# Performance work log

Measured on AMD Instinct MI355X. Metric: run time of the kernel, lower is better.

## Reference

```python
import jax, jax.numpy as jnp
import numpy as np

HEADS = 8
EPS = 1e-12  # F.normalize default eps


def conv1x1(t, w):
    # t: (B, Cin, H, W); w: (Cout, Cin) -> (B, Cout, H, W)
    return jnp.einsum('bchw,oc->bohw', t, w)


def cosine_attn(q, k, v, scale):
    # q: (B,h,d,Nq); k,v: (B,h,d,Nk). Cosine attention: L2-normalize over feature dim d.
    q = q / jnp.maximum(jnp.linalg.norm(q, axis=2, keepdims=True), EPS)
    k = k / jnp.maximum(jnp.linalg.norm(k, axis=2, keepdims=True), EPS)
    attn = jnp.einsum('bhdq,bhdk->bhqk', q, k) * scale
    attn = jax.nn.softmax(attn, axis=-1)
    return jnp.einsum('bhqk,bhdk->bhdq', attn, v)  # (B,h,d,Nq)


def setup_inputs() -> dict:
    key = jax.random.key(0)
    ks = jax.random.split(key, 8)
    B, C, H, W, L = 8, 512, 64, 64, 16
    def w(k, o, i):
        return jax.random.normal(k, (o, i), dtype=jnp.float32) * (1.0 / np.sqrt(i))
    return {
        'x': jax.random.normal(ks[0], (B, C, H, W), dtype=jnp.float32),
        'latents': jax.random.normal(ks[1], (1, C, 1, L), dtype=jnp.float32) * 0.02,
        'w_q_lat': w(ks[2], C, C),
        'w_kv_x': w(ks[3], 2 * C, C),
        'w_q_x': w(ks[4], C, C),
        'w_kv_lat': w(ks[5], 2 * C, C),
        'w_proj': w(ks[6], C, C),
        'b_proj': jnp.zeros((C,), dtype=jnp.float32),
    }


def reference(x, latents, w_q_lat, w_kv_x, w_q_x, w_kv_lat, w_proj, b_proj):
    B, C, H, W = x.shape
    L = latents.shape[-1]
    h = HEADS
    d = C // h
    scale = d ** (-0.5)

    # latents read from spatial features (compression)
    lat = jnp.broadcast_to(latents, (B, C, 1, L))
    ql = conv1x1(lat, w_q_lat).reshape(B, h, d, L)
    kvx = conv1x1(x, w_kv_x)
    kx = kvx[:, :C].reshape(B, h, d, H * W)
    vx = kvx[:, C:].reshape(B, h, d, H * W)
    lat_read = cosine_attn(ql, kx, vx, scale).reshape(B, C, 1, L)

    # latents write back into features (expansion)
    qx = conv1x1(x, w_q_x).reshape(B, h, d, H * W)
    kvl = conv1x1(lat_read, w_kv_lat)
    kl = kvl[:, :C].reshape(B, h, d, L)
    vl = kvl[:, C:].reshape(B, h, d, L)
    x_write = cosine_attn(qx, kl, vl, scale).reshape(B, C, H, W)

    # output projection (dropout p=0 -> identity)
    return conv1x1(x_write, w_proj) + b_proj[None, :, None, None]
```

## Files before the change

kernel.cpp:

```cpp
#include <hip/hip_runtime.h>


typedef __bf16 bf16x8 __attribute__((ext_vector_type(8)));
typedef float floatx4 __attribute__((ext_vector_type(4)));
typedef short short8_t __attribute__((ext_vector_type(8)));
typedef short short4_t __attribute__((ext_vector_type(4)));

#define DEV __device__ __forceinline__

DEV float bf2f(unsigned short u){ union{unsigned int i; float f;} v; v.i = ((unsigned int)u)<<16; return v.f; }
DEV unsigned short f2bf(float f){
  union{float f; unsigned int i;} v; v.f = f;
  unsigned int i = v.i;
  return (unsigned short)((i + 0x7fffu + ((i>>16)&1u)) >> 16);
}

DEV void glds16(const void* g, void* l){
  __builtin_amdgcn_global_load_lds((const __attribute__((address_space(1))) void*)g,
                                   (__attribute__((address_space(3))) void*)l, 16, 0, 0);
}

#define OFF_XT     256ull
#define OFF_KVX    (OFF_XT + 33554432ull)
#define OFF_WKVX   (OFF_KVX + 67108864ull)
#define OFF_WQX    (OFF_WKVX + 1048576ull)
#define OFF_WKVL   (OFF_WQX + 524288ull)
#define OFF_WPROJ  (OFF_WKVL + 1048576ull)
#define OFF_WQLAT  (OFF_WPROJ + 524288ull)
#define OFF_LATF   (OFF_WQLAT + 524288ull)
#define OFF_BIAS   (OFF_LATF + 32768ull)
#define OFF_QLH    (OFF_BIAS + 4096ull)
#define OFF_GNUM   (OFF_QLH + 32768ull)
#define OFF_GDEN   (OFF_GNUM + 524288ull)
#define OFF_KVL    (OFF_GDEN + 4096ull)
#define OFF_KHAT   (OFF_KVL + 524288ull)
#define OFF_GVL    (OFF_KHAT + 524288ull)

__global__ void k_sniff(const unsigned short* __restrict__ x, int* flag){
  int t = threadIdx.x;
  int m = 0;
  for (int i = t; i < 4096; i += 256){ int e = (x[i]>>7)&0xFF; m = (e>m)?e:m; }
  __shared__ int red[256];
  red[t] = m; __syncthreads();
  for (int s = 128; s > 0; s >>= 1){ if (t < s) red[t] = (red[t+s]>red[t])?red[t+s]:red[t]; __syncthreads(); }
  if (t == 0) flag[0] = (red[0] > 150) ? 1 : 0;
}

__global__ __launch_bounds__(256) void k_prep(const void* s0, const void* s1, const void* s2,
                                              const void* s3, const void* s4,
                                              const void* slat, const void* sbias,
                                              unsigned short* __restrict__ wdst,
                                              float* __restrict__ latf, float* __restrict__ biasf,
                                              const int* __restrict__ flag){
  int b = blockIdx.x, t = threadIdx.x;
  int isf = *flag;
  if (b < 896){
    int e = b*2048 + t*8;
    const void* src; int off;
    if (e < 524288)      { src = s0; off = e; }
    else if (e < 786432) { src = s1; off = e - 524288; }
    else if (e < 1310720){ src = s2; off = e - 786432; }
    else if (e < 1572864){ src = s3; off = e - 1310720; }
    else                 { src = s4; off = e - 1572864; }
    if (isf){
      const float* s = (const float*)src + off;
      float4 v0 = *(const float4*)(s);
      float4 v1 = *(const float4*)(s+4);
      unsigned short tmp[8] __attribute__((aligned(16)));
      tmp[0]=f2bf(v0.x); tmp[1]=f2bf(v0.y); tmp[2]=f2bf(v0.z); tmp[3]=f2bf(v0.w);
      tmp[4]=f2bf(v1.x); tmp[5]=f2bf(v1.y); tmp[6]=f2bf(v1.z); tmp[7]=f2bf(v1.w);
      *(short8_t*)&wdst[e] = *(short8_t*)tmp;
    } else {
      *(short8_t*)&wdst[e] = *(const short8_t*)((const unsigned short*)src + off);
    }
  } else if (b < 900){
    int i = (b-896)*2048 + t*8;
#pragma unroll
    for (int j = 0; j < 8; ++j)
      latf[i+j] = isf ? ((const float*)slat)[i+j] : bf2f(((const unsigned short*)slat)[i+j]);
  } else {
    if (t < 512) biasf[t] = isf ? ((const float*)sbias)[t] : bf2f(((const unsigned short*)sbias)[t]);
  }
}

__global__ __launch_bounds__(256) void k_xt(const void* __restrict__ xraw, unsigned short* __restrict__ xT,
                                            const int* __restrict__ flag){
  int nb = blockIdx.x, cb = blockIdx.y, b = blockIdx.z;
  int n0 = nb*64, c0 = cb*64;
  __shared__ unsigned short tile[64][72];
  int t = threadIdx.x;
  if (*flag){
    const float* xp = (const float*)xraw;
#pragma unroll
    for (int i = 0; i < 4; ++i){
      int ch = i*256 + t; int c = ch>>4, n4 = (ch&15)*4;
      float4 v = *(const float4*)&xp[((size_t)(b*512 + c0 + c))*4096 + n0 + n4];
      int cc = n4 ^ (((c>>3)&7)<<3);
      tile[c][cc+0]=f2bf(v.x); tile[c][cc+1]=f2bf(v.y); tile[c][cc+2]=f2bf(v.z); tile[c][cc+3]=f2bf(v.w);
    }
  } else {
    const unsigned short* xp = (const unsigned short*)xraw;
#pragma unroll
    for (int i = 0; i < 2; ++i){
      int ch = i*256 + t; int c = ch>>3, n8 = (ch&7)*8;
      *(short8_t*)&tile[c][n8 ^ (((c>>3)&7)<<3)] =
        *(const short8_t*)&xp[((size_t)(b*512 + c0 + c))*4096 + n0 + n8];
    }
  }
  __syncthreads();
#pragma unroll
  for (int i = 0; i < 2; ++i){
    int ch = i*256 + t; int n = ch>>3, c8 = (ch&7)*8;
    unsigned short tmp[8] __attribute__((aligned(16)));
#pragma unroll
    for (int j = 0; j < 8; ++j){
      int c = c8 + j;
      tmp[j] = tile[c][n ^ (((c>>3)&7)<<3)];
    }
    *(short8_t*)&xT[((size_t)(b*4096 + n0 + n))*512 + c0 + c8] = *(short8_t*)tmp;
  }
}

__global__ __launch_bounds__(256) void k_ql(const unsigned short* __restrict__ wqlat,
                                            const float* __restrict__ latf, float* __restrict__ qlh){
  int h = blockIdx.x, o0 = h*64;
  extern __shared__ char smr[];
  float* latb = (float*)smr;
  unsigned short* wt = (unsigned short*)(smr + 8192);
  float* qbuf = (float*)(smr + 8192 + 17408);
  float* rinv = (float*)(smr + 8192 + 17408 + 4096);
  int t = threadIdx.x;
  int o = t>>2, l4 = (t&3)*4;
  float acc[4] = {0.f,0.f,0.f,0.f};
  for (int kk = 0; kk < 512; kk += 128){
    __syncthreads();
#pragma unroll
    for (int j = 0; j < 8; ++j){ int i = j*256 + t; latb[i] = latf[kk*16 + i]; }
#pragma unroll
    for (int j = 0; j < 4; ++j){ int ch = j*256 + t; int r = ch>>4, kc = (ch&15)*8;
      *(short8_t*)&wt[r*136 + kc] = *(const short8_t*)&wqlat[(size_t)(o0+r)*512 + kk + kc]; }
    __syncthreads();
    for (int k = 0; k < 128; ++k){
      float w = bf2f(wt[o*136 + k]);
      const float* lr = &latb[k*16 + l4];
#pragma unroll
      for (int j = 0; j < 4; ++j) acc[j] += w*lr[j];
    }
  }
#pragma unroll
  for (int j = 0; j < 4; ++j) qbuf[o*16 + l4 + j] = acc[j];
  __syncthreads();
  if (t < 16){
    float ss = 0.f;
    for (int oo = 0; oo < 64; ++oo){ float v = qbuf[oo*16 + t]; ss += v*v; }
    rinv[t] = 0.125f / fmaxf(sqrtf(ss), 1e-12f);
  }
  __syncthreads();
#pragma unroll
  for (int j = 0; j < 4; ++j) qlh[(h*16 + l4 + j)*64 + o] = acc[j]*rinv[l4 + j];
}

DEV void gemm128(const unsigned short* __restrict__ Ap0, const unsigned short* __restrict__ Ap1,
                 const unsigned short* __restrict__ Bp,
                 unsigned short* At, unsigned short* Bt, floatx4 (&acc)[4][4]){
  int t = threadIdx.x, lane = t&63, wave = t>>6;
  int wm = wave>>1, wn = wave&1, lr = lane&15, lq = lane>>4;
  int rsub = lane>>3;
  int koff = ((lane&7) ^ rsub)*8;
  int sw = lr&7;
  for (int kk = 0; kk < 512; kk += 64){
    __syncthreads();
#pragma unroll
    for (int c2 = 0; c2 < 4; ++c2){
      int chunk = wave*4 + c2;
      int row = chunk*8 + rsub;
      const unsigned short* gp = (chunk < 8) ? (Ap0 + (size_t)row*512 + kk + koff)
                                             : (Ap1 + (size_t)(row-64)*512 + kk + koff);
      glds16(gp, At + chunk*512);
    }
#pragma unroll
    for (int c2 = 0; c2 < 4; ++c2){
      int chunk = wave*4 + c2;
      int row = chunk*8 + rsub;
      glds16(Bp + (size_t)row*512 + kk + koff, Bt + chunk*512);
    }
    __syncthreads();
#pragma unroll
    for (int ks = 0; ks < 2; ++ks){
      int vo = ((ks*4 + lq) ^ sw)*8;
      bf16x8 a[4], b[4];
#pragma unroll
      for (int mt = 0; mt < 4; ++mt) a[mt] = *(const bf16x8*)&At[(wm*64 + mt*16 + lr)*64 + vo];
#pragma unroll
      for (int nt = 0; nt < 4; ++nt) b[nt] = *(const bf16x8*)&Bt[(wn*64 + nt*16 + lr)*64 + vo];
#pragma unroll
      for (int mt = 0; mt < 4; ++mt)
#pragma unroll
        for (int nt = 0; nt < 4; ++nt)
          acc[mt][nt] = __builtin_amdgcn_mfma_f32_16x16x32_bf16(a[mt], b[nt], acc[mt][nt], 0, 0, 0);
    }
  }
  __syncthreads();
}

__global__ __launch_bounds__(256) void k_kvattn1(const unsigned short* __restrict__ wkvx,
                                                 const unsigned short* __restrict__ xT,
                                                 const float* __restrict__ qlh2,
                                                 float* __restrict__ gnum, float* __restrict__ gden){
  int nb = blockIdx.x, h = blockIdx.y, b = blockIdx.z;
  int n0 = nb*128;
  extern __shared__ char smr[];
  unsigned short* At  = (unsigned short*)smr;
  unsigned short* Bt  = (unsigned short*)(smr + 16384);
  unsigned short* kt  = (unsigned short*)smr;
  unsigned short* vt  = (unsigned short*)(smr + 18432);
  unsigned short* qls = (unsigned short*)(smr + 35840);
  float* ssq  = (float*)(smr + 38144);
  float* wred = (float*)(smr + 38656);
  unsigned short* pt  = (unsigned short*)(smr + 38912);
  int t = threadIdx.x, lane = t&63, wave = t>>6;
  int wm = wave>>1, wn = wave&1, lr = lane&15, lq = lane>>4;
  for (int i = t; i < 1024; i += 256) qls[(i>>6)*72 + (i&63)] = f2bf(qlh2[(size_t)h*1024 + i]);
  floatx4 acc[4][4];
  floatx4 zero = {0.f,0.f,0.f,0.f};
#pragma unroll
  for (int i = 0; i < 4; ++i) for (int j = 0; j < 4; ++j) acc[i][j] = zero;
  gemm128(wkvx + (size_t)(h*64)*512, wkvx + (size_t)(512 + h*64)*512,
          xT + ((size_t)(b*4096 + n0))*512, At, Bt, acc);
  if (wm == 0){
#pragma unroll
    for (int nt = 0; nt < 4; ++nt){
      float s = 0.f;
#pragma unroll
      for (int mt = 0; mt < 4; ++mt)
#pragma unroll
        for (int r = 0; r < 4; ++r) s += acc[mt][nt][r]*acc[mt][nt][r];
      s += __shfl_xor(s, 16); s += __shfl_xor(s, 32);
      if (lq == 0) ssq[wn*64 + nt*16 + lr] = 1.f / fmaxf(sqrtf(s), 1e-12f);
    }
  } else {
#pragma unroll
    for (int mt = 0; mt < 4; ++mt)
#pragma unroll
      for (int nt = 0; nt < 4; ++nt){
        int col = wn*64 + nt*16 + lr;
#pragma unroll
        for (int r = 0; r < 4; ++r) vt[(mt*16 + lq*4 + r)*136 + col] = f2bf(acc[mt][nt][r]);
      }
  }
  __syncthreads();
  if (wm == 0){
#pragma unroll
    for (int nt = 0; nt < 4; ++nt){
      int col = wn*64 + nt*16 + lr;
      float rinv = ssq[col];
#pragma unroll
      for (int mt = 0; mt < 4; ++mt){
        unsigned short tmp[4] __attribute__((aligned(8)));
#pragma unroll
        for (int r = 0; r < 4; ++r) tmp[r] = f2bf(acc[mt][nt][r]*rinv);
        *(short4_t*)&kt[col*72 + mt*16 + lq*4] = *(short4_t*)tmp;
      }
    }
  }
  __syncthreads();
  floatx4 sl[2]; sl[0] = zero; sl[1] = zero;
#pragma unroll
  for (int ks = 0; ks < 2; ++ks){
    bf16x8 bb = *(const bf16x8*)&qls[lr*72 + ks*32 + lq*8];
#pragma unroll
    for (int i = 0; i < 2; ++i){
      bf16x8 aa = *(const bf16x8*)&kt[((wave*2 + i)*16 + lr)*72 + ks*32 + lq*8];
      sl[i] = __builtin_amdgcn_mfma_f32_16x16x32_bf16(aa, bb, sl[i], 0, 0, 0);
    }
  }
  float dp = 0.f;
  float pv[2][4];
#pragma unroll
  for (int i = 0; i < 2; ++i)
#pragma unroll
    for (int r = 0; r < 4; ++r){ float p = __expf(sl[i][r]); pv[i][r] = p; dp += p; }
  dp += __shfl_xor(dp, 16); dp += __shfl_xor(dp, 32);
  if (lq == 0) wred[wave*16 + lr] = dp;
#pragma unroll
  for (int i = 0; i < 2; ++i){
    unsigned short tmp[4] __attribute__((aligned(8)));
#pragma unroll
    for (int r = 0; r < 4; ++r) tmp[r] = f2bf(pv[i][r]);
    *(short4_t*)&pt[lr*136 + (wave*2 + i)*16 + lq*4] = *(short4_t*)tmp;
  }
  __syncthreads();
  int bh = b*8 + h;
  if (t < 16) atomicAdd(&gden[bh*16 + t], wred[t] + wred[16+t] + wred[32+t] + wred[48+t]);
  floatx4 nacc = zero;
#pragma unroll
  for (int ks = 0; ks < 4; ++ks){
    bf16x8 aa = *(const bf16x8*)&vt[(wave*16 + lr)*136 + ks*32 + lq*8];
    bf16x8 bb = *(const bf16x8*)&pt[lr*136 + ks*32 + lq*8];
    nacc = __builtin_amdgcn_mfma_f32_16x16x32_bf16(aa, bb, nacc, 0, 0, 0);
  }
  float* gp = &gnum[((size_t)bh*16 + lr)*64 + wave*16 + lq*4];
#pragma unroll
  for (int r = 0; r < 4; ++r) atomicAdd(&gp[r], nacc[r]);
}

__global__ __launch_bounds__(256) void k_kvl(const unsigned short* __restrict__ wkvl,
                                             const float* __restrict__ gnum, const float* __restrict__ gden,
                                             float* __restrict__ kvl){
  int ob = blockIdx.x, b = blockIdx.y;
  extern __shared__ char smr[];
  float* latb = (float*)smr;
  unsigned short* wt = (unsigned short*)(smr + 32768);
  int t = threadIdx.x;
  for (int i = t; i < 8192; i += 256){
    int c = i>>4, l = i&15;
    int h = c>>6, d = c&63;
    int bh = b*8 + h;
    latb[i] = gnum[((size_t)(bh*16 + l))*64 + d] / gden[bh*16 + l];
  }
  int o = t>>4, l = t&15;
  int o0 = ob*16;
  float acc = 0.f;
  for (int kk = 0; kk < 512; kk += 128){
    __syncthreads();
    { int r = t>>4, kc = (t&15)*8;
      *(short8_t*)&wt[r*136 + kc] = *(const short8_t*)&wkvl[(size_t)(o0+r)*512 + kk + kc]; }
    __syncthreads();
    for (int k = 0; k < 128; ++k) acc += bf2f(wt[o*136 + k]) * latb[(kk+k)*16 + l];
  }
  kvl[((size_t)(b*1024 + o0 + o))*16 + l] = acc;
}

__global__ void k_klnorm(const float* __restrict__ kvl, float* __restrict__ khat, float* __restrict__ gvl){
  int l = blockIdx.x, h = blockIdx.y, b = blockIdx.z, d = threadIdx.x;
  float kl = kvl[((size_t)(b*1024 + h*64 + d))*16 + l];
  float vl = kvl[((size_t)(b*1024 + 512 + h*64 + d))*16 + l];
  float ss = kl*kl;
  for (int off = 32; off; off >>= 1) ss += __shfl_xor(ss, off);
  float inv = 0.125f / fmaxf(sqrtf(ss), 1e-12f);
  size_t o = ((size_t)((b*8+h)*16 + l))*64 + d;
  khat[o] = kl*inv;
  gvl[o] = vl;
}

__global__ __launch_bounds__(256) void k_mmat(const unsigned short* __restrict__ wproj,
                                              const float* __restrict__ gvl,
                                              unsigned short* __restrict__ Mg){
  int cb = blockIdx.x, h = blockIdx.y, b = blockIdx.z;
  __shared__ unsigned short wt[128*68];
  int t = threadIdx.x;
#pragma unroll
  for (int i = 0; i < 4; ++i){ int ch = i*256 + t; int c = ch>>3, d8 = (ch&7)*8;
    *(short8_t*)&wt[c*68 + d8] = *(const short8_t*)&wproj[(size_t)(cb*128 + c)*512 + h*64 + d8]; }
  int l = t&15, cq = t>>4;
  float v[64];
  const float* vp = &gvl[((size_t)(b*8+h)*16 + l)*64];
#pragma unroll
  for (int j = 0; j < 16; ++j){ float4 f = *(const float4*)&vp[j*4];
    v[j*4+0]=f.x; v[j*4+1]=f.y; v[j*4+2]=f.z; v[j*4+3]=f.w; }
  __syncthreads();
#pragma unroll
  for (int c8 = 0; c8 < 8; ++c8){
    int c = cq*8 + c8;
    float dot = 0.f;
#pragma unroll
    for (int d = 0; d < 64; ++d) dot += bf2f(wt[c*68 + d]) * v[d];
    Mg[((size_t)(b*512) + cb*128 + c)*128 + h*16 + l] = f2bf(dot);
  }
}

__global__ __launch_bounds__(256) void k_attn2p2(const unsigned short* __restrict__ wqx,
                                                 const unsigned short* __restrict__ xT,
                                                 const float* __restrict__ khatg,
                                                 unsigned short* __restrict__ Pg){
  int nb = blockIdx.x, hp = blockIdx.y, b = blockIdx.z;
  int n0 = nb*128;
  extern __shared__ char smr[];
  unsigned short* At  = (unsigned short*)smr;
  unsigned short* Bt  = (unsigned short*)(smr + 16384);
  unsigned short* qt0 = (unsigned short*)smr;
  unsigned short* qt1 = (unsigned short*)(smr + 18432);
  unsigned short* khs = (unsigned short*)(smr + 36864);
  float* ssq = (float*)(smr + 41472);
  int t = threadIdx.x, lane = t&63, wave = t>>6;
  int wm = wave>>1, wn = wave&1, lr = lane&15, lq = lane>>4;
  for (int i = t; i < 2048; i += 256){
    int hh = i>>10, rem = i&1023;
    khs[hh*1152 + (rem>>6)*72 + (rem&63)] = f2bf(khatg[((size_t)(b*8 + hp*2 + hh))*1024 + rem]);
  }
  floatx4 acc[4][4];
  floatx4 zero = {0.f,0.f,0.f,0.f};
#pragma unroll
  for (int i = 0; i < 4; ++i) for (int j = 0; j < 4; ++j) acc[i][j] = zero;
  gemm128(wqx + (size_t)(hp*128)*512, wqx + (size_t)(hp*128 + 64)*512,
          xT + ((size_t)(b*4096 + n0))*512, At, Bt, acc);
#pragma unroll
  for (int nt = 0; nt < 4; ++nt){
    float s = 0.f;
#pragma unroll
    for (int mt = 0; mt < 4; ++mt)
#pragma unroll
      for (int r = 0; r < 4; ++r) s += acc[mt][nt][r]*acc[mt][nt][r];
    s += __shfl_xor(s, 16); s += __shfl_xor(s, 32);
    if (lq == 0) ssq[wm*128 + wn*64 + nt*16 + lr] = 1.f / fmaxf(sqrtf(s), 1e-12f);
  }
  __syncthreads();
  unsigned short* qtr = wm ? qt1 : qt0;
#pragma unroll
  for (int nt = 0; nt < 4; ++nt){
    int col = wn*64 + nt*16 + lr;
    float rinv = ssq[wm*128 + col];
#pragma unroll
    for (int mt = 0; mt < 4; ++mt){
      unsigned short tmp[4] __attribute__((aligned(8)));
#pragma unroll
      for (int r = 0; r < 4; ++r) tmp[r] = f2bf(acc[mt][nt][r]*rinv);
      *(short4_t*)&qtr[col*72 + mt*16 + lq*4] = *(short4_t*)tmp;
    }
  }
  __syncthreads();
  floatx4 sl[4];
#pragma unroll
  for (int i = 0; i < 4; ++i) sl[i] = zero;
  unsigned short* qsrc = wm ? qt1 : qt0;
#pragma unroll
  for (int ks = 0; ks < 2; ++ks){
    bf16x8 bb = *(const bf16x8*)&khs[wm*1152 + lr*72 + ks*32 + lq*8];
#pragma unroll
    for (int i = 0; i < 4; ++i){
      bf16x8 aa = *(const bf16x8*)&qsrc[((wn*4 + i)*16 + lr)*72 + ks*32 + lq*8];
      sl[i] = __builtin_amdgcn_mfma_f32_16x16x32_bf16(aa, bb, sl[i], 0, 0, 0);
    }
  }
  int h = hp*2 + wm;
#pragma unroll
  for (int i = 0; i < 4; ++i){
    float p[4], s[4];
#pragma unroll
    for (int r = 0; r < 4; ++r){ p[r] = __expf(sl[i][r]); s[r] = p[r]; }
#pragma unroll
    for (int r = 0; r < 4; ++r){
      s[r] += __shfl_xor(s[r], 1);
      s[r] += __shfl_xor(s[r], 2);
      s[r] += __shfl_xor(s[r], 4);
      s[r] += __shfl_xor(s[r], 8);
    }
    int nbase = wn*64 + i*16 + lq*4;
#pragma unroll
    for (int r = 0; r < 4; ++r)
      Pg[((size_t)(b*4096 + n0 + nbase + r))*128 + h*16 + lr] = f2bf(p[r]/s[r]);
  }
}

__global__ __launch_bounds__(256) void k_out(const unsigned short* __restrict__ Mg,
                                             const unsigned short* __restrict__ Pg,
                                             const float* __restrict__ biasf,
                                             void* __restrict__ outv, const int* __restrict__ flag){
  int nb = blockIdx.x, cb = blockIdx.y, b = blockIdx.z;
  int n0 = nb*128, c0 = cb*64;
  extern __shared__ char smr[];
  unsigned short* At = (unsigned short*)smr;
  unsigned short* Bt = At + 64*136;
  int t = threadIdx.x, lane = t&63, wave = t>>6;
  int wm = wave>>1, wn = wave&1, lr = lane&15, lq = lane>>4;
#pragma unroll
  for (int i = 0; i < 4; ++i){ int ch = i*256 + t; int r = ch>>4, p8 = (ch&15)*8;
    *(short8_t*)&At[r*136 + p8] = *(const short8_t*)&Mg[((size_t)(b*512 + c0 + r))*128 + p8]; }
#pragma unroll
  for (int i = 0; i < 8; ++i){ int ch = i*256 + t; int r = ch>>4, p8 = (ch&15)*8;
    *(short8_t*)&Bt[r*136 + p8] = *(const short8_t*)&Pg[((size_t)(b*4096 + n0 + r))*128 + p8]; }
  __syncthreads();
  floatx4 acc[2][4];
  floatx4 zero = {0.f,0.f,0.f,0.f};
#pragma unroll
  for (int i = 0; i < 2; ++i) for (int j = 0; j < 4; ++j) acc[i][j] = zero;
#pragma unroll
  for (int ks = 0; ks < 4; ++ks){
    bf16x8 a0 = *(const bf16x8*)&At[(wm*32 + lr)*136 + ks*32 + lq*8];
    bf16x8 a1 = *(const bf16x8*)&At[(wm*32 + 16 + lr)*136 + ks*32 + lq*8];
#pragma unroll
    for (int nt = 0; nt < 4; ++nt){
      bf16x8 bb = *(const bf16x8*)&Bt[(wn*64 + nt*16 + lr)*136 + ks*32 + lq*8];
      acc[0][nt] = __builtin_amdgcn_mfma_f32_16x16x32_bf16(a0, bb, acc[0][nt], 0, 0, 0);
      acc[1][nt] = __builtin_amdgcn_mfma_f32_16x16x32_bf16(a1, bb, acc[1][nt], 0, 0, 0);
    }
  }
  __syncthreads();
  float* ct = (float*)smr;
#pragma unroll
  for (int mt = 0; mt < 2; ++mt)
#pragma unroll
    for (int nt = 0; nt < 4; ++nt)
#pragma unroll
      for (int r = 0; r < 4; ++r){
        int row = wm*32 + mt*16 + lq*4 + r;
        ct[row*132 + wn*64 + nt*16 + lr] = acc[mt][nt][r] + biasf[c0 + row];
      }
  __syncthreads();
  if (*flag){
    float* of = (float*)outv;
#pragma unroll
    for (int i = 0; i < 8; ++i){ int ch = i*256 + t; int r = ch>>5, c4 = (ch&31)*4;
      *(float4*)&of[((size_t)(b*512 + c0 + r))*4096 + n0 + c4] = *(float4*)&ct[r*132 + c4]; }
  } else {
    unsigned short* ob = (unsigned short*)outv;
#pragma unroll
    for (int i = 0; i < 4; ++i){ int ch = i*256 + t; int r = ch>>4, c8 = (ch&15)*8;
      unsigned short tmp[8] __attribute__((aligned(16)));
#pragma unroll
      for (int j = 0; j < 8; ++j) tmp[j] = f2bf(ct[r*132 + c8 + j]);
      *(short8_t*)&ob[((size_t)(b*512 + c0 + r))*4096 + n0 + c8] = *(short8_t*)tmp; }
  }
}

extern "C" void kernel_launch(void* const* d_in, const int* in_sizes, int n_in,
                              void* d_out, int out_size, void* d_ws, size_t ws_size,
                              hipStream_t stream){
  (void)in_sizes; (void)n_in; (void)out_size; (void)ws_size;
  char* ws = (char*)d_ws;
  int* flag              = (int*)ws;
  unsigned short* xT     = (unsigned short*)(ws + OFF_XT);
  unsigned short* Pg     = (unsigned short*)(ws + OFF_KVX);
  unsigned short* Mg     = (unsigned short*)(ws + OFF_KVX + 8388608ull);
  unsigned short* wkvx   = (unsigned short*)(ws + OFF_WKVX);
  unsigned short* wqx    = (unsigned short*)(ws + OFF_WQX);
  unsigned short* wkvl   = (unsigned short*)(ws + OFF_WKVL);
  unsigned short* wproj  = (unsigned short*)(ws + OFF_WPROJ);
  float* latf  = (float*)(ws + OFF_LATF);
  float* biasf = (float*)(ws + OFF_BIAS);
  float* qlh   = (float*)(ws + OFF_QLH);
  float* gnum  = (float*)(ws + OFF_GNUM);
  float* gden  = (float*)(ws + OFF_GDEN);
  float* kvl   = (float*)(ws + OFF_KVL);
  float* khat  = (float*)(ws + OFF_KHAT);
  float* gvl   = (float*)(ws + OFF_GVL);

  k_sniff<<<1, 256, 0, stream>>>((const unsigned short*)d_in[0], flag);

  k_prep<<<901, 256, 0, stream>>>(d_in[3], d_in[4], d_in[5], d_in[6], d_in[2],
                                  d_in[1], d_in[7], wkvx, latf, biasf, flag);

  k_xt<<<dim3(64, 8, 8), 256, 0, stream>>>(d_in[0], xT, flag);

  k_ql<<<8, 256, 8192 + 17408 + 4096 + 64, stream>>>((unsigned short*)(ws + OFF_WQLAT), latf, qlh);

  hipMemsetAsync(ws + OFF_GNUM, 0, 524288 + 4096, stream);

  k_kvattn1<<<dim3(32, 8, 8), 256, 43264, stream>>>(wkvx, xT, qlh, gnum, gden);
  k_kvl<<<dim3(64, 8), 256, 32768 + 16*136*2, stream>>>(wkvl, gnum, gden, kvl);
  k_klnorm<<<dim3(16, 8, 8), 64, 0, stream>>>(kvl, khat, gvl);
  k_mmat<<<dim3(4, 8, 8), 256, 0, stream>>>(wproj, gvl, Mg);
  k_attn2p2<<<dim3(32, 4, 8), 256, 42496, stream>>>(wqx, xT, khat, Pg);
  k_out<<<dim3(32, 8, 8), 256, 52224, stream>>>(Mg, Pg, biasf, d_out, flag);
}
```

Baseline: 298.4 us.

## Process two heads per block in kvattn1 to reuse the loaded x tile

The K/V projection-plus-attention kernel now handles two heads per block with 512 threads and a 256-row weight tile, so each x tile loaded into shared memory feeds twice as many output rows. The per-head attention epilogue becomes a loop over the two heads, with the norm computed in-register instead of through a shared buffer. The block count halves and shared memory per block grows, which may lower occupancy. f2bf is also switched to the compiler's native bf16 conversion.

```diff
diff --git a/kernel.cpp b/kernel.cpp
--- a/kernel.cpp
+++ b/kernel.cpp
@@ -10,9 +10,8 @@
 
 DEV float bf2f(unsigned short u){ union{unsigned int i; float f;} v; v.i = ((unsigned int)u)<<16; return v.f; }
 DEV unsigned short f2bf(float f){
-  union{float f; unsigned int i;} v; v.f = f;
-  unsigned int i = v.i;
-  return (unsigned short)((i + 0x7fffu + ((i>>16)&1u)) >> 16);
+  __bf16 h = (__bf16)f;
+  unsigned short u; __builtin_memcpy(&u, &h, 2); return u;
 }
 
 DEV void glds16(const void* g, void* l){
@@ -203,105 +202,148 @@
   __syncthreads();
 }
 
-__global__ __launch_bounds__(256) void k_kvattn1(const unsigned short* __restrict__ wkvx,
+DEV void gemm256(const unsigned short* __restrict__ Ap0, const unsigned short* __restrict__ Ap1,
+                 const unsigned short* __restrict__ Bp,
+                 unsigned short* At, unsigned short* Bt, floatx4 (&acc)[4][4]){
+  int t = threadIdx.x, lane = t&63, wave = t>>6;
+  int wm = wave>>1, wn = wave&1, lr = lane&15, lq = lane>>4;
+  int rsub = lane>>3;
+  int koff = ((lane&7) ^ rsub)*8;
+  int sw = lr&7;
+  for (int kk = 0; kk < 512; kk += 64){
+    __syncthreads();
+#pragma unroll
+    for (int c2 = 0; c2 < 4; ++c2){
+      int chunk = wave*4 + c2;
+      int row = (chunk&15)*8 + rsub;
+      const unsigned short* gp = (chunk < 16) ? (Ap0 + (size_t)row*512 + kk + koff)
+                                              : (Ap1 + (size_t)row*512 + kk + koff);
+      glds16(gp, At + chunk*512);
+    }
+#pragma unroll
+    for (int c2 = 0; c2 < 2; ++c2){
+      int chunk = wave*2 + c2;
+      int row = chunk*8 + rsub;
+      glds16(Bp + (size_t)row*512 + kk + koff, Bt + chunk*512);
+    }
+    __syncthreads();
+#pragma unroll
+    for (int ks = 0; ks < 2; ++ks){
+      int vo = ((ks*4 + lq) ^ sw)*8;
+      bf16x8 a[4], b[4];
+#pragma unroll
+      for (int mt = 0; mt < 4; ++mt) a[mt] = *(const bf16x8*)&At[(wm*64 + mt*16 + lr)*64 + vo];
+#pragma unroll
+      for (int nt = 0; nt < 4; ++nt) b[nt] = *(const bf16x8*)&Bt[(wn*64 + nt*16 + lr)*64 + vo];
+#pragma unroll
+      for (int mt = 0; mt < 4; ++mt)
+#pragma unroll
+        for (int nt = 0; nt < 4; ++nt)
+          acc[mt][nt] = __builtin_amdgcn_mfma_f32_16x16x32_bf16(a[mt], b[nt], acc[mt][nt], 0, 0, 0);
+    }
+  }
+  __syncthreads();
+}
+
+__global__ __launch_bounds__(512) void k_kvattn1(const unsigned short* __restrict__ wkvx,
                                                  const unsigned short* __restrict__ xT,
                                                  const float* __restrict__ qlh2,
                                                  float* __restrict__ gnum, float* __restrict__ gden){
-  int nb = blockIdx.x, h = blockIdx.y, b = blockIdx.z;
+  int nb = blockIdx.x, hp = blockIdx.y, b = blockIdx.z;
   int n0 = nb*128;
   extern __shared__ char smr[];
   unsigned short* At  = (unsigned short*)smr;
-  unsigned short* Bt  = (unsigned short*)(smr + 16384);
+  unsigned short* Bt  = (unsigned short*)(smr + 32768);
   unsigned short* kt  = (unsigned short*)smr;
   unsigned short* vt  = (unsigned short*)(smr + 18432);
-  unsigned short* qls = (unsigned short*)(smr + 35840);
-  float* ssq  = (float*)(smr + 38144);
-  float* wred = (float*)(smr + 38656);
-  unsigned short* pt  = (unsigned short*)(smr + 38912);
+  unsigned short* pt  = (unsigned short*)(smr + 35840);
+  unsigned short* qls = (unsigned short*)(smr + 49152);
+  float* wred = (float*)(smr + 53760);
   int t = threadIdx.x, lane = t&63, wave = t>>6;
   int wm = wave>>1, wn = wave&1, lr = lane&15, lq = lane>>4;
-  for (int i = t; i < 1024; i += 256) qls[(i>>6)*72 + (i&63)] = f2bf(qlh2[(size_t)h*1024 + i]);
+  for (int i = t; i < 2048; i += 512){
+    int hh = i>>10, rem = i&1023;
+    qls[hh*1152 + (rem>>6)*72 + (rem&63)] = f2bf(qlh2[((size_t)(hp*2+hh))*1024 + rem]);
+  }
   floatx4 acc[4][4];
   floatx4 zero = {0.f,0.f,0.f,0.f};
 #pragma unroll
   for (int i = 0; i < 4; ++i) for (int j = 0; j < 4; ++j) acc[i][j] = zero;
-  gemm128(wkvx + (size_t)(h*64)*512, wkvx + (size_t)(512 + h*64)*512,
+  gemm256(wkvx + (size_t)(hp*128)*512, wkvx + (size_t)(512 + hp*128)*512,
           xT + ((size_t)(b*4096 + n0))*512, At, Bt, acc);
-  if (wm == 0){
-#pragma unroll
-    for (int nt = 0; nt < 4; ++nt){
+#pragma unroll
+  for (int hh = 0; hh < 2; ++hh){
+    if (hh) __syncthreads();
+    if (wm == hh){
+#pragma unroll
+      for (int nt = 0; nt < 4; ++nt){
+        float s = 0.f;
+#pragma unroll
+        for (int mt = 0; mt < 4; ++mt)
+#pragma unroll
+          for (int r = 0; r < 4; ++r) s += acc[mt][nt][r]*acc[mt][nt][r];
+        s += __shfl_xor(s, 16); s += __shfl_xor(s, 32);
+        float rinv = 1.f / fmaxf(sqrtf(s), 1e-12f);
+        int col = wn*64 + nt*16 + lr;
+#pragma unroll
+        for (int mt = 0; mt < 4; ++mt){
+          unsigned short tmp[4] __attribute__((aligned(8)));
+#pragma unroll
+          for (int r = 0; r < 4; ++r) tmp[r] = f2bf(acc[mt][nt][r]*rinv);
+          *(short4_t*)&kt[col*72 + mt*16 + lq*4] = *(short4_t*)tmp;
+        }
+      }
+    } else if (wm == 2 + hh){
+#pragma unroll
+      for (int mt = 0; mt < 4; ++mt)
+#pragma unroll
+        for (int nt = 0; nt < 4; ++nt){
+          int col = wn*64 + nt*16 + lr;
+#pragma unroll
+          for (int r = 0; r < 4; ++r) vt[(mt*16 + lq*4 + r)*136 + col] = f2bf(acc[mt][nt][r]);
+        }
+    }
+    __syncthreads();
+    floatx4 sl = zero;
+#pragma unroll
+    for (int ks = 0; ks < 2; ++ks){
+      bf16x8 bb = *(const bf16x8*)&qls[hh*1152 + lr*72 + ks*32 + lq*8];
+      bf16x8 aa = *(const bf16x8*)&kt[(wave*16 + lr)*72 + ks*32 + lq*8];
+      sl = __builtin_amdgcn_mfma_f32_16x16x32_bf16(aa, bb, sl, 0, 0, 0);
+    }
+    float dp = 0.f;
+    float pv[4];
+#pragma unroll
+    for (int r = 0; r < 4; ++r){ float p = __expf(sl[r]); pv[r] = p; dp += p; }
+    dp += __shfl_xor(dp, 16); dp += __shfl_xor(dp, 32);
+    if (lq == 0) wred[wave*16 + lr] = dp;
+    {
+      unsigned short tmp[4] __attribute__((aligned(8)));
+#pragma unroll
+      for (int r = 0; r < 4; ++r) tmp[r] = f2bf(pv[r]);
+      *(short4_t*)&pt[lr*136 + wave*16 + lq*4] = *(short4_t*)tmp;
+    }
+    __syncthreads();
+    int bh = b*8 + hp*2 + hh;
+    if (t < 16){
       float s = 0.f;
 #pragma unroll
-      for (int mt = 0; mt < 4; ++mt)
-#pragma unroll
-        for (int r = 0; r < 4; ++r) s += acc[mt][nt][r]*acc[mt][nt][r];
-      s += __shfl_xor(s, 16); s += __shfl_xor(s, 32);
-      if (lq == 0) ssq[wn*64 + nt*16 + lr] = 1.f / fmaxf(sqrtf(s), 1e-12f);
-    }
-  } else {
-#pragma unroll
-    for (int mt = 0; mt < 4; ++mt)
-#pragma unroll
-      for (int nt = 0; nt < 4; ++nt){
-        int col = wn*64 + nt*16 + lr;
-#pragma unroll
-        for (int r = 0; r < 4; ++r) vt[(mt*16 + lq*4 + r)*136 + col] = f2bf(acc[mt][nt][r]);
+      for (int w = 0; w < 8; ++w) s += wred[w*16 + t];
+      atomicAdd(&gden[bh*16 + t], s);
+    }
+    if (wave < 4){
+      floatx4 nacc = zero;
+#pragma unroll
+      for (int ks = 0; ks < 4; ++ks){
+        bf16x8 aa = *(const bf16x8*)&vt[(wave*16 + lr)*136 + ks*32 + lq*8];
+        bf16x8 bb = *(const bf16x8*)&pt[lr*136 + ks*32 + lq*8];
+        nacc = __builtin_amdgcn_mfma_f32_16x16x32_bf16(aa, bb, nacc, 0, 0, 0);
       }
-  }
-  __syncthreads();
-  if (wm == 0){
-#pragma unroll
-    for (int nt = 0; nt < 4; ++nt){
-      int col = wn*64 + nt*16 + lr;
-      float rinv = ssq[col];
-#pragma unroll
-      for (int mt = 0; mt < 4; ++mt){
-        unsigned short tmp[4] __attribute__((aligned(8)));
-#pragma unroll
-        for (int r = 0; r < 4; ++r) tmp[r] = f2bf(acc[mt][nt][r]*rinv);
-        *(short4_t*)&kt[col*72 + mt*16 + lq*4] = *(short4_t*)tmp;
-      }
-    }
-  }
-  __syncthreads();
-  floatx4 sl[2]; sl[0] = zero; sl[1] = zero;
-#pragma unroll
-  for (int ks = 0; ks < 2; ++ks){
-    bf16x8 bb = *(const bf16x8*)&qls[lr*72 + ks*32 + lq*8];
-#pragma unroll
-    for (int i = 0; i < 2; ++i){
-      bf16x8 aa = *(const bf16x8*)&kt[((wave*2 + i)*16 + lr)*72 + ks*32 + lq*8];
-      sl[i] = __builtin_amdgcn_mfma_f32_16x16x32_bf16(aa, bb, sl[i], 0, 0, 0);
-    }
-  }
-  float dp = 0.f;
-  float pv[2][4];
-#pragma unroll
-  for (int i = 0; i < 2; ++i)
-#pragma unroll
-    for (int r = 0; r < 4; ++r){ float p = __expf(sl[i][r]); pv[i][r] = p; dp += p; }
-  dp += __shfl_xor(dp, 16); dp += __shfl_xor(dp, 32);
-  if (lq == 0) wred[wave*16 + lr] = dp;
-#pragma unroll
-  for (int i = 0; i < 2; ++i){
-    unsigned short tmp[4] __attribute__((aligned(8)));
-#pragma unroll
-    for (int r = 0; r < 4; ++r) tmp[r] = f2bf(pv[i][r]);
-    *(short4_t*)&pt[lr*136 + (wave*2 + i)*16 + lq*4] = *(short4_t*)tmp;
-  }
-  __syncthreads();
-  int bh = b*8 + h;
-  if (t < 16) atomicAdd(&gden[bh*16 + t], wred[t] + wred[16+t] + wred[32+t] + wred[48+t]);
-  floatx4 nacc = zero;
-#pragma unroll
-  for (int ks = 0; ks < 4; ++ks){
-    bf16x8 aa = *(const bf16x8*)&vt[(wave*16 + lr)*136 + ks*32 + lq*8];
-    bf16x8 bb = *(const bf16x8*)&pt[lr*136 + ks*32 + lq*8];
-    nacc = __builtin_amdgcn_mfma_f32_16x16x32_bf16(aa, bb, nacc, 0, 0, 0);
-  }
-  float* gp = &gnum[((size_t)bh*16 + lr)*64 + wave*16 + lq*4];
-#pragma unroll
-  for (int r = 0; r < 4; ++r) atomicAdd(&gp[r], nacc[r]);
+      float* gp = &gnum[((size_t)bh*16 + lr)*64 + wave*16 + lq*4];
+#pragma unroll
+      for (int r = 0; r < 4; ++r) atomicAdd(&gp[r], nacc[r]);
+    }
+  }
 }
 
 __global__ __launch_bounds__(256) void k_kvl(const unsigned short* __restrict__ wkvl,
@@ -546,7 +588,7 @@
 
   hipMemsetAsync(ws + OFF_GNUM, 0, 524288 + 4096, stream);
 
-  k_kvattn1<<<dim3(32, 8, 8), 256, 43264, stream>>>(wkvx, xT, qlh, gnum, gden);
+  k_kvattn1<<<dim3(32, 4, 8), 512, 54272, stream>>>(wkvx, xT, qlh, gnum, gden);
   k_kvl<<<dim3(64, 8), 256, 32768 + 16*136*2, stream>>>(wkvl, gnum, gden, kvl);
   k_klnorm<<<dim3(16, 8, 8), 64, 0, stream>>>(kvl, khat, gvl);
   k_mmat<<<dim3(4, 8, 8), 256, 0, stream>>>(wproj, gvl, Mg);
```

Result: no change. 300.0 us (+0.5%).
